# Performance work log

Measured on AMD Instinct MI355X. Metric: run time of the kernel, lower is better.

## Reference

```python
import jax, jax.numpy as jnp
import numpy as np

B, N, D_IN, D_OUT, NUM_RING = 32, 8192, 64, 128, 4
BN_EPS = 1e-5


def setup_inputs() -> dict:
    key = jax.random.key(0)
    ks = jax.random.split(key, 8)
    return {
        "x": jax.random.normal(ks[0], (B, D_IN, N), dtype=jnp.float32),
        "ring": jax.random.randint(ks[1], (B, N), 0, NUM_RING, dtype=jnp.int64),
        "W": jax.random.normal(ks[2], (NUM_RING, D_OUT, D_IN), dtype=jnp.float32) * 0.1,
        "b": jax.random.normal(ks[3], (NUM_RING, D_OUT), dtype=jnp.float32) * 0.1,
        "gamma": jax.random.uniform(ks[4], (NUM_RING, D_OUT), dtype=jnp.float32) + 0.5,
        "beta": jax.random.normal(ks[5], (NUM_RING, D_OUT), dtype=jnp.float32) * 0.1,
        "mean": jax.random.normal(ks[6], (NUM_RING, D_OUT), dtype=jnp.float32) * 0.1,
        "var": jax.random.uniform(ks[7], (NUM_RING, D_OUT), dtype=jnp.float32) + 0.5,
    }


def reference(x, ring, W, b, gamma, beta, mean, var):
    # x: [B, 64, N]; ring: [B, N] int labels in [0, num_ring)
    xt = jnp.transpose(x, (0, 2, 1))  # [B, N, 64]
    Bv, Nv, _ = xt.shape
    num_ring = W.shape[0]
    out = jnp.zeros((Bv, Nv, W.shape[1]), dtype=x.dtype)
    neg = jnp.finfo(x.dtype).min
    for i in range(num_ring):  # small fixed loop over rings
        # 1x1 conv == per-point linear, then BatchNorm (inference-mode affine)
        y = jnp.einsum("bnd,od->bno", xt, W[i]) + b[i]  # [B, N, 128]
        scale = gamma[i] * jax.lax.rsqrt(var[i] + BN_EPS)
        y = (y - mean[i]) * scale + beta[i]
        m = (ring == i)[..., None]  # [B, N, 1]
        # per-(batch, ring) segment max over points, broadcast back to members
        ymax = jnp.max(jnp.where(m, y, neg), axis=1, keepdims=True)  # [B, 1, 128]
        out = jnp.where(m, ymax, out)
    return jnp.transpose(out, (0, 2, 1))  # [B, 128, N]
```

## Files before the change

### kernel.cpp

```cpp
#include <hip/hip_runtime.h>
#include <cstdint>
#include <cstddef>

#define BB 32
#define NN 8192
#define DIN 64
#define DOUT 128
#define NR 4
#define BN_EPS 1e-5f

#define SEGS 16

typedef float nfloat4 __attribute__((ext_vector_type(4)));
typedef float floatx4 __attribute__((ext_vector_type(4)));
typedef short short8 __attribute__((ext_vector_type(8)));
typedef unsigned short ushort8 __attribute__((ext_vector_type(8)));

#define WS_KEYS_OFF 512
#define WS_BUCKETS_OFF 66560

__device__ inline unsigned short f2bf(float f) {
  const unsigned int u = __float_as_uint(f);
  return (unsigned short)((u + 0x7fffu + ((u >> 16) & 1u)) >> 16);
}

__global__ void k_bucket(const int* __restrict__ ring, int* __restrict__ counts,
                         unsigned short* __restrict__ buckets) {
  const int b = blockIdx.y;
  const int n0 = blockIdx.x * 1024;
  const int lane = threadIdx.x & 63;
#pragma unroll
  for (int k = 0; k < 4; ++k) {
    const int n = n0 + k * 256 + (int)threadIdx.x;
    const int r = ring[b * NN + n];
    unsigned long long mym = 0ull;
#pragma unroll
    for (int rr = 0; rr < NR; ++rr) {
      unsigned long long mr = __ballot(r == rr);
      if (r == rr) mym = mr;
    }
    const int leader = __ffsll((unsigned long long)mym) - 1;
    const int cnt = __popcll(mym);
    const int pos_in = __popcll(mym & ((1ull << lane) - 1ull));
    int base = 0;
    if (lane == leader) base = atomicAdd(&counts[b * NR + r], cnt);
    base = __shfl(base, leader, 64);
    buckets[(b * NR + r) * NN + base + pos_in] = (unsigned short)n;
  }
}

__global__ void __launch_bounds__(256) k_transpose(const float* __restrict__ x,
                                                   unsigned short* __restrict__ xt) {
  const int b = blockIdx.y;
  const int n0 = blockIdx.x * 256;
  __shared__ float tile[DIN * 256];
  const int wave = threadIdx.x >> 6;
  const int lane = threadIdx.x & 63;
#pragma unroll
  for (int d = wave; d < DIN; d += 4) {
    const float4 v =
        *(const float4*)&x[((size_t)b * DIN + d) * NN + n0 + lane * 4];
    *(float4*)&tile[d * 256 + lane * 4] = v;
  }
  __syncthreads();
  const int p = (int)threadIdx.x;
  unsigned short* dst = xt + ((size_t)b * NN + n0 + p) * DIN;
#pragma unroll
  for (int j = 0; j < 8; ++j) {
    ushort8 v;
#pragma unroll
    for (int i = 0; i < 8; ++i) v[i] = f2bf(tile[(8 * j + i) * 256 + p]);
    *(ushort8*)&dst[8 * j] = v;
  }
}

__global__ void __launch_bounds__(256) k_compute(
    const unsigned short* __restrict__ xt, const float* __restrict__ W,
    const int* __restrict__ counts, const unsigned short* __restrict__ buckets,
    unsigned int* __restrict__ smax_keys) {
  const int seg = blockIdx.x;
  const int r = blockIdx.y;
  const int b = blockIdx.z;
  const int wave = (int)threadIdx.x >> 6;
  const int lane = (int)threadIdx.x & 63;
  const int quad = lane >> 4;
  const int l16 = lane & 15;
  const int count = counts[b * NR + r];
  if (count == 0) return;
  const unsigned short* bk = buckets + (size_t)(b * NR + r) * NN;
  const unsigned short* xb = xt + (size_t)b * NN * DIN;

  short8 af[2][2];
#pragma unroll
  for (int tt = 0; tt < 2; ++tt) {
    const int chan = (wave + 4 * tt) * 16 + l16;
    const float* wr = W + ((size_t)r * DOUT + chan) * DIN + quad * 8;
#pragma unroll
    for (int ks = 0; ks < 2; ++ks) {
      const float4 w0 = *(const float4*)&wr[ks * 32];
      const float4 w1 = *(const float4*)&wr[ks * 32 + 4];
      short8 a;
      a[0] = (short)f2bf(w0.x); a[1] = (short)f2bf(w0.y);
      a[2] = (short)f2bf(w0.z); a[3] = (short)f2bf(w0.w);
      a[4] = (short)f2bf(w1.x); a[5] = (short)f2bf(w1.y);
      a[6] = (short)f2bf(w1.z); a[7] = (short)f2bf(w1.w);
      af[tt][ks] = a;
    }
  }

  floatx4 rmax0 = {-INFINITY, -INFINITY, -INFINITY, -INFINITY};
  floatx4 rmax1 = rmax0;

  const int tiles = (count + 15) >> 4;
  for (int T = seg; T < tiles; T += SEGS) {
    int s = T * 16 + l16;
    if (s > count - 1) s = count - 1;
    const int n = bk[s];
    const unsigned short* xr = xb + (size_t)n * DIN + quad * 8;
    const short8 b0 = *(const short8*)&xr[0];
    const short8 b1 = *(const short8*)&xr[32];
    floatx4 acc0 = {0.f, 0.f, 0.f, 0.f};
    floatx4 acc1 = {0.f, 0.f, 0.f, 0.f};
    acc0 = __builtin_amdgcn_mfma_f32_16x16x32_bf16(af[0][0], b0, acc0, 0, 0, 0);
    acc0 = __builtin_amdgcn_mfma_f32_16x16x32_bf16(af[0][1], b1, acc0, 0, 0, 0);
    acc1 = __builtin_amdgcn_mfma_f32_16x16x32_bf16(af[1][0], b0, acc1, 0, 0, 0);
    acc1 = __builtin_amdgcn_mfma_f32_16x16x32_bf16(af[1][1], b1, acc1, 0, 0, 0);
#pragma unroll
    for (int p = 0; p < 4; ++p) {
      rmax0[p] = fmaxf(rmax0[p], acc0[p]);
      rmax1[p] = fmaxf(rmax1[p], acc1[p]);
    }
  }

#pragma unroll
  for (int tt = 0; tt < 2; ++tt) {
#pragma unroll
    for (int p = 0; p < 4; ++p) {
      float v = (tt == 0) ? rmax0[p] : rmax1[p];
      v = fmaxf(v, __shfl_xor(v, 1, 64));
      v = fmaxf(v, __shfl_xor(v, 2, 64));
      v = fmaxf(v, __shfl_xor(v, 4, 64));
      v = fmaxf(v, __shfl_xor(v, 8, 64));
      if (l16 == 0) {
        const int chan = (wave + 4 * tt) * 16 + quad * 4 + p;
        const unsigned int u = __float_as_uint(v);
        const unsigned int key = (u & 0x80000000u) ? ~u : (u | 0x80000000u);
        atomicMax(&smax_keys[(size_t)(b * NR + r) * DOUT + chan], key);
      }
    }
  }
}

__global__ void k_out(const float* __restrict__ bias, const float* __restrict__ gamma,
                      const float* __restrict__ beta, const float* __restrict__ mean,
                      const float* __restrict__ var, const int* __restrict__ ring,
                      const unsigned int* __restrict__ smax_keys,
                      float* __restrict__ out) {
  const int b = blockIdx.z;
  const int og = blockIdx.y;
  const int n0 = blockIdx.x * 1024;

  __shared__ float ymax[32 * NR];
  if (threadIdx.x < 32 * NR) {
    const int oo = (int)threadIdx.x >> 2;
    const int r = (int)threadIdx.x & 3;
    const int o = og * 32 + oo;
    const int t = r * DOUT + o;
    const unsigned int key = smax_keys[(size_t)b * NR * DOUT + t];
    const unsigned int u = (key & 0x80000000u) ? (key ^ 0x80000000u) : ~key;
    const float raw = __uint_as_float(u);
    const float sc = gamma[t] * rsqrtf(var[t] + BN_EPS);
    ymax[oo * NR + r] = (raw + bias[t] - mean[t]) * sc + beta[t];
  }
  __syncthreads();

  const int n = n0 + (int)threadIdx.x * 4;
  const int4 rg = *(const int4*)&ring[(size_t)b * NN + n];
#pragma unroll 8
  for (int oo = 0; oo < 32; ++oo) {
    const int o = og * 32 + oo;
    nfloat4 v;
    v.x = ymax[oo * NR + rg.x];
    v.y = ymax[oo * NR + rg.y];
    v.z = ymax[oo * NR + rg.z];
    v.w = ymax[oo * NR + rg.w];
    __builtin_nontemporal_store(v, (nfloat4*)&out[((size_t)b * DOUT + o) * NN + n]);
  }
}

extern "C" void kernel_launch(void* const* d_in, const int* in_sizes, int n_in,
                              void* d_out, int out_size, void* d_ws, size_t ws_size,
                              hipStream_t stream) {
  const float* x = (const float*)d_in[0];
  const int* ring = (const int*)d_in[1];
  const float* W = (const float*)d_in[2];
  const float* bias = (const float*)d_in[3];
  const float* gamma = (const float*)d_in[4];
  const float* beta = (const float*)d_in[5];
  const float* mean = (const float*)d_in[6];
  const float* var = (const float*)d_in[7];
  float* out = (float*)d_out;

  char* ws = (char*)d_ws;
  int* counts = (int*)(ws + 0);
  unsigned int* keys = (unsigned int*)(ws + WS_KEYS_OFF);
  unsigned short* buckets = (unsigned short*)(ws + WS_BUCKETS_OFF);
  unsigned short* xt = (unsigned short*)d_out;

  (void)hipMemsetAsync(ws, 0, WS_KEYS_OFF + (size_t)BB * NR * DOUT * 4, stream);

  k_bucket<<<dim3(NN / 1024, BB), 256, 0, stream>>>(ring, counts, buckets);
  k_transpose<<<dim3(NN / 256, BB), 256, 0, stream>>>(x, xt);
  k_compute<<<dim3(SEGS, NR, BB), 256, 0, stream>>>(xt, W, counts, buckets, keys);
  k_out<<<dim3(NN / 1024, DOUT / 32, BB), 256, 0, stream>>>(bias, gamma, beta, mean,
                                                            var, ring, keys, out);
}
```

Measured before the change: 259.5 us.

## Fuse transpose and bucketing into compute, evaluating all rings densely per point

Removes the bucketing and transpose kernels and the scattered gather. The compute kernel now reads x directly in its native [B,64,N] layout, converts to bf16 in registers, and runs the MFMA for all four rings on every point. Each result is masked by the point's ring label before the running max. This trades four times the matrix work and strided column reads for fewer launches, no intermediate bf16 buffer, and coalesced access without indirection. Each block now issues atomics for all four rings, so atomicMax traffic on the keys buffer grows as well.

New measurement: 230.4 us. 1.13x faster.

```diff
diff --git a/kernel.cpp b/kernel.cpp
--- a/kernel.cpp
+++ b/kernel.cpp
@@ -1,4 +1,5 @@
 #include <hip/hip_runtime.h>
+#include <hip/hip_bf16.h>
 #include <cstdint>
 #include <cstddef>
 
@@ -9,143 +10,120 @@
 #define NR 4
 #define BN_EPS 1e-5f
 
-#define SEGS 16
-
 typedef float nfloat4 __attribute__((ext_vector_type(4)));
 typedef float floatx4 __attribute__((ext_vector_type(4)));
 typedef short short8 __attribute__((ext_vector_type(8)));
-typedef unsigned short ushort8 __attribute__((ext_vector_type(8)));
 
-#define WS_KEYS_OFF 512
-#define WS_BUCKETS_OFF 66560
 
 __device__ inline unsigned short f2bf(float f) {
   const unsigned int u = __float_as_uint(f);
   return (unsigned short)((u + 0x7fffu + ((u >> 16) & 1u)) >> 16);
 }
 
-__global__ void k_bucket(const int* __restrict__ ring, int* __restrict__ counts,
-                         unsigned short* __restrict__ buckets) {
-  const int b = blockIdx.y;
-  const int n0 = blockIdx.x * 1024;
-  const int lane = threadIdx.x & 63;
-#pragma unroll
-  for (int k = 0; k < 4; ++k) {
-    const int n = n0 + k * 256 + (int)threadIdx.x;
-    const int r = ring[b * NN + n];
-    unsigned long long mym = 0ull;
-#pragma unroll
-    for (int rr = 0; rr < NR; ++rr) {
-      unsigned long long mr = __ballot(r == rr);
-      if (r == rr) mym = mr;
-    }
-    const int leader = __ffsll((unsigned long long)mym) - 1;
-    const int cnt = __popcll(mym);
-    const int pos_in = __popcll(mym & ((1ull << lane) - 1ull));
-    int base = 0;
-    if (lane == leader) base = atomicAdd(&counts[b * NR + r], cnt);
-    base = __shfl(base, leader, 64);
-    buckets[(b * NR + r) * NN + base + pos_in] = (unsigned short)n;
-  }
-}
-
-__global__ void __launch_bounds__(256) k_transpose(const float* __restrict__ x,
-                                                   unsigned short* __restrict__ xt) {
-  const int b = blockIdx.y;
-  const int n0 = blockIdx.x * 256;
-  __shared__ float tile[DIN * 256];
-  const int wave = threadIdx.x >> 6;
-  const int lane = threadIdx.x & 63;
-#pragma unroll
-  for (int d = wave; d < DIN; d += 4) {
-    const float4 v =
-        *(const float4*)&x[((size_t)b * DIN + d) * NN + n0 + lane * 4];
-    *(float4*)&tile[d * 256 + lane * 4] = v;
-  }
-  __syncthreads();
-  const int p = (int)threadIdx.x;
-  unsigned short* dst = xt + ((size_t)b * NN + n0 + p) * DIN;
-#pragma unroll
-  for (int j = 0; j < 8; ++j) {
-    ushort8 v;
-#pragma unroll
-    for (int i = 0; i < 8; ++i) v[i] = f2bf(tile[(8 * j + i) * 256 + p]);
-    *(ushort8*)&dst[8 * j] = v;
-  }
+__device__ inline void pack2(float a, float b, short8& dst, int idx) {
+  __hip_bfloat162 h = __float22bfloat162_rn(make_float2(a, b));
+  const unsigned int bits = *(unsigned int*)&h;
+  dst[idx] = (short)(bits & 0xffffu);
+  dst[idx + 1] = (short)(bits >> 16);
 }
 
 __global__ void __launch_bounds__(256) k_compute(
-    const unsigned short* __restrict__ xt, const float* __restrict__ W,
-    const int* __restrict__ counts, const unsigned short* __restrict__ buckets,
-    unsigned int* __restrict__ smax_keys) {
-  const int seg = blockIdx.x;
-  const int r = blockIdx.y;
-  const int b = blockIdx.z;
+    const float* __restrict__ x, const float* __restrict__ W,
+    const int* __restrict__ ring, unsigned int* __restrict__ smax_keys) {
+  const int b = blockIdx.y;
+  const int n0 = blockIdx.x * 256;
   const int wave = (int)threadIdx.x >> 6;
   const int lane = (int)threadIdx.x & 63;
   const int quad = lane >> 4;
   const int l16 = lane & 15;
-  const int count = counts[b * NR + r];
-  if (count == 0) return;
-  const unsigned short* bk = buckets + (size_t)(b * NR + r) * NN;
-  const unsigned short* xb = xt + (size_t)b * NN * DIN;
+  const float* xb = x + (size_t)b * DIN * NN;
+  const int* rgb = ring + (size_t)b * NN;
 
   short8 af[2][2];
 #pragma unroll
   for (int tt = 0; tt < 2; ++tt) {
     const int chan = (wave + 4 * tt) * 16 + l16;
-    const float* wr = W + ((size_t)r * DOUT + chan) * DIN + quad * 8;
+    const float* wr = W + ((size_t)blockIdx.z * 0 + 0);
+    (void)wr;
+  }
+
+  floatx4 rmax[2][NR];
 #pragma unroll
-    for (int ks = 0; ks < 2; ++ks) {
-      const float4 w0 = *(const float4*)&wr[ks * 32];
-      const float4 w1 = *(const float4*)&wr[ks * 32 + 4];
-      short8 a;
-      a[0] = (short)f2bf(w0.x); a[1] = (short)f2bf(w0.y);
-      a[2] = (short)f2bf(w0.z); a[3] = (short)f2bf(w0.w);
-      a[4] = (short)f2bf(w1.x); a[5] = (short)f2bf(w1.y);
-      a[6] = (short)f2bf(w1.z); a[7] = (short)f2bf(w1.w);
-      af[tt][ks] = a;
+  for (int tt = 0; tt < 2; ++tt)
+#pragma unroll
+    for (int r = 0; r < NR; ++r) rmax[tt][r] = {-INFINITY, -INFINITY, -INFINITY, -INFINITY};
+
+  short8 afr[NR][2][2];
+#pragma unroll
+  for (int r = 0; r < NR; ++r) {
+#pragma unroll
+    for (int tt = 0; tt < 2; ++tt) {
+      const int chan = (wave + 4 * tt) * 16 + l16;
+      const float* wr = W + ((size_t)r * DOUT + chan) * DIN + quad * 8;
+#pragma unroll
+      for (int ks = 0; ks < 2; ++ks) {
+        const float4 w0 = *(const float4*)&wr[ks * 32];
+        const float4 w1 = *(const float4*)&wr[ks * 32 + 4];
+        short8 a;
+        pack2(w0.x, w0.y, a, 0);
+        pack2(w0.z, w0.w, a, 2);
+        pack2(w1.x, w1.y, a, 4);
+        pack2(w1.z, w1.w, a, 6);
+        afr[r][tt][ks] = a;
+      }
     }
   }
 
-  floatx4 rmax0 = {-INFINITY, -INFINITY, -INFINITY, -INFINITY};
-  floatx4 rmax1 = rmax0;
-
-  const int tiles = (count + 15) >> 4;
-  for (int T = seg; T < tiles; T += SEGS) {
-    int s = T * 16 + l16;
-    if (s > count - 1) s = count - 1;
-    const int n = bk[s];
-    const unsigned short* xr = xb + (size_t)n * DIN + quad * 8;
-    const short8 b0 = *(const short8*)&xr[0];
-    const short8 b1 = *(const short8*)&xr[32];
-    floatx4 acc0 = {0.f, 0.f, 0.f, 0.f};
-    floatx4 acc1 = {0.f, 0.f, 0.f, 0.f};
-    acc0 = __builtin_amdgcn_mfma_f32_16x16x32_bf16(af[0][0], b0, acc0, 0, 0, 0);
-    acc0 = __builtin_amdgcn_mfma_f32_16x16x32_bf16(af[0][1], b1, acc0, 0, 0, 0);
-    acc1 = __builtin_amdgcn_mfma_f32_16x16x32_bf16(af[1][0], b0, acc1, 0, 0, 0);
-    acc1 = __builtin_amdgcn_mfma_f32_16x16x32_bf16(af[1][1], b1, acc1, 0, 0, 0);
+#pragma unroll 1
+  for (int T = 0; T < 16; ++T) {
+    const int n = n0 + T * 16 + l16;
+    const int rr = rgb[n];
+    float bx[8], by[8];
 #pragma unroll
-    for (int p = 0; p < 4; ++p) {
-      rmax0[p] = fmaxf(rmax0[p], acc0[p]);
-      rmax1[p] = fmaxf(rmax1[p], acc1[p]);
+    for (int j = 0; j < 8; ++j) {
+      bx[j] = xb[(size_t)(quad * 8 + j) * NN + n];
+      by[j] = xb[(size_t)(32 + quad * 8 + j) * NN + n];
+    }
+    short8 b0, b1;
+#pragma unroll
+    for (int j = 0; j < 4; ++j) {
+      pack2(bx[2 * j], bx[2 * j + 1], b0, 2 * j);
+      pack2(by[2 * j], by[2 * j + 1], b1, 2 * j);
+    }
+#pragma unroll
+    for (int r = 0; r < NR; ++r) {
+      floatx4 acc0 = {0.f, 0.f, 0.f, 0.f};
+      floatx4 acc1 = {0.f, 0.f, 0.f, 0.f};
+      acc0 = __builtin_amdgcn_mfma_f32_16x16x32_bf16(afr[r][0][0], b0, acc0, 0, 0, 0);
+      acc0 = __builtin_amdgcn_mfma_f32_16x16x32_bf16(afr[r][0][1], b1, acc0, 0, 0, 0);
+      acc1 = __builtin_amdgcn_mfma_f32_16x16x32_bf16(afr[r][1][0], b0, acc1, 0, 0, 0);
+      acc1 = __builtin_amdgcn_mfma_f32_16x16x32_bf16(afr[r][1][1], b1, acc1, 0, 0, 0);
+      const bool m = (rr == r);
+#pragma unroll
+      for (int p = 0; p < 4; ++p) {
+        rmax[0][r][p] = fmaxf(rmax[0][r][p], m ? acc0[p] : -INFINITY);
+        rmax[1][r][p] = fmaxf(rmax[1][r][p], m ? acc1[p] : -INFINITY);
+      }
     }
   }
 
 #pragma unroll
   for (int tt = 0; tt < 2; ++tt) {
 #pragma unroll
-    for (int p = 0; p < 4; ++p) {
-      float v = (tt == 0) ? rmax0[p] : rmax1[p];
-      v = fmaxf(v, __shfl_xor(v, 1, 64));
-      v = fmaxf(v, __shfl_xor(v, 2, 64));
-      v = fmaxf(v, __shfl_xor(v, 4, 64));
-      v = fmaxf(v, __shfl_xor(v, 8, 64));
-      if (l16 == 0) {
-        const int chan = (wave + 4 * tt) * 16 + quad * 4 + p;
-        const unsigned int u = __float_as_uint(v);
-        const unsigned int key = (u & 0x80000000u) ? ~u : (u | 0x80000000u);
-        atomicMax(&smax_keys[(size_t)(b * NR + r) * DOUT + chan], key);
+    for (int r = 0; r < NR; ++r) {
+#pragma unroll
+      for (int p = 0; p < 4; ++p) {
+        float v = rmax[tt][r][p];
+        v = fmaxf(v, __shfl_xor(v, 1, 64));
+        v = fmaxf(v, __shfl_xor(v, 2, 64));
+        v = fmaxf(v, __shfl_xor(v, 4, 64));
+        v = fmaxf(v, __shfl_xor(v, 8, 64));
+        if (l16 == 0) {
+          const int chan = (wave + 4 * tt) * 16 + quad * 4 + p;
+          const unsigned int u = __float_as_uint(v);
+          const unsigned int key = (u & 0x80000000u) ? ~u : (u | 0x80000000u);
+          atomicMax(&smax_keys[(size_t)(b * NR + r) * DOUT + chan], key);
+        }
       }
     }
   }
@@ -201,17 +179,11 @@
   const float* var = (const float*)d_in[7];
   float* out = (float*)d_out;
 
-  char* ws = (char*)d_ws;
-  int* counts = (int*)(ws + 0);
-  unsigned int* keys = (unsigned int*)(ws + WS_KEYS_OFF);
-  unsigned short* buckets = (unsigned short*)(ws + WS_BUCKETS_OFF);
-  unsigned short* xt = (unsigned short*)d_out;
+  unsigned int* keys = (unsigned int*)d_ws;
 
-  (void)hipMemsetAsync(ws, 0, WS_KEYS_OFF + (size_t)BB * NR * DOUT * 4, stream);
+  (void)hipMemsetAsync(keys, 0, (size_t)BB * NR * DOUT * 4, stream);
 
-  k_bucket<<<dim3(NN / 1024, BB), 256, 0, stream>>>(ring, counts, buckets);
-  k_transpose<<<dim3(NN / 256, BB), 256, 0, stream>>>(x, xt);
-  k_compute<<<dim3(SEGS, NR, BB), 256, 0, stream>>>(xt, W, counts, buckets, keys);
+  k_compute<<<dim3(NN / 256, BB), 256, 0, stream>>>(x, W, ring, keys);
   k_out<<<dim3(NN / 1024, DOUT / 32, BB), 256, 0, stream>>>(bias, gamma, beta, mean,
                                                             var, ring, keys, out);
 }
```
